# Performance work log

Hardware: AMD Instinct MI355X
Metric: run time of the kernel (lower is better)

The kernel has to match this reference:

```python
import jax, jax.numpy as jnp
import numpy as np

# video grid and attention geometry (must match init_kwargs)
F_T, H_T, W_T = 4, 32, 32
K = 3                      # kernel_size (odd)
P = K // 2
T = F_T * H_T * W_T        # max_num_tokens = 4096
HEADS = 8
DIM_HEAD = 64
SCALE = DIM_HEAD ** -0.5
DIM = 512
INNER = HEADS * DIM_HEAD


def _build_window_indices():
    # flat token index grid, padded with sentinel T (out-of-range -> zero row after gather)
    idx = np.arange(T).reshape(F_T, H_T, W_T)
    padded = np.full((F_T + 2 * P, H_T + 2 * P, W_T + 2 * P), T, dtype=np.int64)
    padded[P:P + F_T, P:P + H_T, P:P + W_T] = idx
    # [T, K^3] neighborhood indices, kernel offsets in (kf, kh, kw) C-order (matches unfoldNd)
    win = np.lib.stride_tricks.sliding_window_view(padded, (K, K, K)).reshape(T, K ** 3)
    # causal: mask keys whose flat index is strictly in the future of the query
    causal = np.arange(T)[:, None] < win
    causal = np.concatenate([np.zeros((T, 1), dtype=bool), causal], axis=1)  # BOS column never masked
    return jnp.asarray(win), jnp.asarray(causal)

WIN_IDX, CAUSAL_MASK = _build_window_indices()


def setup_inputs() -> dict:
    key = jax.random.key(0)
    k0, k1, k2, k3 = jax.random.split(key, 4)
    n = T  # 1 BOS + (T-1) video tokens; padding logic pads body to exactly T tokens
    x = jax.random.normal(k0, (2, n, DIM), dtype=jnp.float32)
    Wq = jax.random.normal(k1, (DIM, INNER), dtype=jnp.float32) * (DIM ** -0.5)
    Wkv = jax.random.normal(k2, (DIM, 2 * INNER), dtype=jnp.float32) * (DIM ** -0.5)
    Wo = jax.random.normal(k3, (INNER, DIM), dtype=jnp.float32) * (INNER ** -0.5)
    bo = jnp.zeros((DIM,), dtype=jnp.float32)
    return {"x": x, "Wq": Wq, "Wkv": Wkv, "Wo": Wo, "bo": bo}


def _split_heads(t, b):
    # [b, n, h*d] -> [(b*h), n, d]
    n = t.shape[1]
    return t.reshape(b, n, HEADS, DIM_HEAD).transpose(0, 2, 1, 3).reshape(b * HEADS, n, DIM_HEAD)


def reference(x, Wq, Wkv, Wo, bo):
    b, n, _ = x.shape
    tpf = H_T * W_T
    padding = tpf - (n - 1) % tpf  # pads body tokens to a multiple of tokens_per_frame
    x = jnp.pad(x, ((0, 0), (0, padding), (0, 0)))
    q = x @ Wq
    k, v = jnp.split(x @ Wkv, 2, axis=-1)
    q, k, v = (_split_heads(t, b) for t in (q, k, v))
    bh = b * HEADS
    q = q[:, 1:] * SCALE            # drop BOS query; [bh, T, d]
    bos_v = v[:, :1]                # BOS attends only to itself -> its value passes through
    k_bos, k = k[:, :1], k[:, 1:]
    v_bos, v = v[:, :1], v[:, 1:]
    # gather K^3 3D neighborhoods; sentinel index T maps to a zero row
    zero_row = jnp.zeros((bh, 1, DIM_HEAD), dtype=k.dtype)
    k_nb = jnp.concatenate([k, zero_row], axis=1)[:, WIN_IDX]   # [bh, T, K^3, d]
    v_nb = jnp.concatenate([v, zero_row], axis=1)[:, WIN_IDX]
    # prepend global BOS key/value to every window
    k_nb = jnp.concatenate([jnp.broadcast_to(k_bos[:, :, None], (bh, T, 1, DIM_HEAD)), k_nb], axis=2)
    v_nb = jnp.concatenate([jnp.broadcast_to(v_bos[:, :, None], (bh, T, 1, DIM_HEAD)), v_nb], axis=2)
    sim = jnp.einsum('bid,bijd->bij', q, k_nb)                  # [bh, T, K^3+1]
    sim = jnp.where(CAUSAL_MASK[None], -jnp.finfo(sim.dtype).max, sim)
    attn = jax.nn.softmax(sim, axis=-1)
    out = jnp.einsum('bij,bijd->bid', attn, v_nb)               # [bh, T, d]
    out = jnp.concatenate([bos_v, out], axis=1)                 # [bh, T+1, d]
    np_tok = out.shape[1]
    out = out.reshape(b, HEADS, np_tok, DIM_HEAD).transpose(0, 2, 1, 3).reshape(b, np_tok, INNER)
    return (out @ Wo + bo)[:, :n]
```

## Files before the change

kernel.cpp:

```cpp
#include <hip/hip_runtime.h>


#define T_TOK   4096
#define DIM     512
#define NQKV    1536

typedef unsigned short u16;
typedef unsigned int   u32;
typedef unsigned long long u64;
typedef __attribute__((ext_vector_type(8))) short short8;
typedef __attribute__((ext_vector_type(4))) float f32x4;

__device__ __forceinline__ u16 f2bf(float f) {
    u32 u = __float_as_uint(f);
    return (u16)((u + 0x7fffu + ((u >> 16) & 1u)) >> 16);
}
__device__ __forceinline__ float b2f(u16 u) {
    return __uint_as_float(((u32)u) << 16);
}

__device__ __forceinline__ void gload_lds16(const void* g, void* l) {
    __builtin_amdgcn_global_load_lds(
        (const __attribute__((address_space(1))) void*)g,
        (__attribute__((address_space(3))) void*)l, 16, 0, 0);
}

__global__ void cast_all_kernel(const float4* __restrict__ x,
                                const float* __restrict__ Wq, const float* __restrict__ Wkv,
                                const float* __restrict__ Wo,
                                u16* __restrict__ xb, u16* __restrict__ Wt,
                                u16* __restrict__ Wot) {
    __shared__ float S[64 * 65];
    int blk = blockIdx.x;
    int tid = threadIdx.x;
    if (blk < 4096) {
        int i = blk * 256 + tid;
        float4 v = x[i];
        u64 pack = (u64)f2bf(v.x) | ((u64)f2bf(v.y) << 16) |
                   ((u64)f2bf(v.z) << 32) | ((u64)f2bf(v.w) << 48);
        ((u64*)xb)[i] = pack;
        return;
    }
    int isWo = blk >= 4288;
    int tIdx = isWo ? (blk - 4288) : (blk - 4096);
    int tn = tIdx >> 3, tk = tIdx & 7;
    #pragma unroll
    for (int p = 0; p < 16; ++p) {
        int kl = p * 4 + (tid >> 6), nl = tid & 63;
        int gk = tk * 64 + kl, gn = tn * 64 + nl;
        float v;
        if (isWo)            v = Wo[gk * 512 + gn];
        else if (gn < 512)   v = Wq[gk * 512 + gn];
        else                 v = Wkv[gk * 1024 + (gn - 512)];
        S[kl * 65 + nl] = v;
    }
    __syncthreads();
    u16* dst = isWo ? Wot : Wt;
    #pragma unroll
    for (int p = 0; p < 16; ++p) {
        int nl = p * 4 + (tid >> 6), kl = tid & 63;
        dst[(size_t)(tn * 64 + nl) * 512 + tk * 64 + kl] = f2bf(S[kl * 65 + nl]);
    }
}

template <int BM, int BN, int MODE>
__global__ __launch_bounds__(256)
void gemm_nt(const u16* __restrict__ A, const u16* __restrict__ B,
             void* __restrict__ Cv, const float* __restrict__ bias,
             int lda, int ldb, int ldc) {
    constexpr int K = 512, BK = 32;
    constexpr int ACH = BM * 4;
    constexpr int NCH = (BM + BN) * 4;
    constexpr int NLD = NCH / 256;
    constexpr int ABYTES = BM * 64;
    constexpr int MI = BM / 32, NJ = BN / 32;
    __shared__ __align__(16) char lds[(BM + BN) * 64];
    const int tid  = threadIdx.x;
    const int lane = tid & 63, wave = tid >> 6;
    const int quad = lane >> 4, mrow = lane & 15;
    const int wm = wave >> 1, wn = wave & 1;
    const int bm = blockIdx.y, bn = blockIdx.x;

    const char* gptr[NLD];
    char*       lptr[NLD];
    #pragma unroll
    for (int it = 0; it < NLD; ++it) {
        int c   = it * 256 + tid;
        int inB = (c >= ACH);
        int a   = inB ? c - ACH : c;
        int r   = a >> 2;
        int kc  = ((a & 3) - (r >> 1)) & 3;
        int row = (inB ? bn * BN : bm * BM) + r;
        const u16* base = inB ? B : A;
        int ld = inB ? ldb : lda;
        gptr[it] = (const char*)(base + (size_t)row * ld + kc * 8);
        lptr[it] = (char*)lds + (it * 256 + wave * 64) * 16;
    }
    const short8* aLds[MI];
    const short8* bLds[NJ];
    #pragma unroll
    for (int i = 0; i < MI; ++i) {
        int ra = wm * (BM / 2) + i * 16 + mrow;
        aLds[i] = (const short8*)(lds + (ra * 4 + ((quad + (ra >> 1)) & 3)) * 16);
    }
    #pragma unroll
    for (int j = 0; j < NJ; ++j) {
        int rb = wn * (BN / 2) + j * 16 + mrow;
        bLds[j] = (const short8*)(lds + ABYTES + (rb * 4 + ((quad + (rb >> 1)) & 3)) * 16);
    }

    f32x4 acc[MI][NJ] = {};
    for (int k0 = 0; k0 < K; k0 += BK) {
        #pragma unroll
        for (int it = 0; it < NLD; ++it)
            gload_lds16(gptr[it] + 2 * k0, lptr[it]);
        __syncthreads();
        short8 af[MI], bf[NJ];
        #pragma unroll
        for (int i = 0; i < MI; ++i) af[i] = *aLds[i];
        #pragma unroll
        for (int j = 0; j < NJ; ++j) bf[j] = *bLds[j];
        #pragma unroll
        for (int i = 0; i < MI; ++i)
            #pragma unroll
            for (int j = 0; j < NJ; ++j)
                acc[i][j] = __builtin_amdgcn_mfma_f32_16x16x32_bf16(af[i], bf[j], acc[i][j], 0, 0, 0);
        __syncthreads();
    }

    #pragma unroll
    for (int i = 0; i < MI; ++i) {
        #pragma unroll
        for (int j = 0; j < NJ; ++j) {
            int colg = bn * BN + wn * (BN / 2) + j * 16 + mrow;
            #pragma unroll
            for (int r = 0; r < 4; ++r) {
                int rowg = bm * BM + wm * (BM / 2) + i * 16 + quad * 4 + r;
                if (MODE == 0) {
                    ((u16*)Cv)[(size_t)rowg * ldc + colg] = f2bf(acc[i][j][r]);
                } else {
                    ((float*)Cv)[(size_t)rowg * ldc + colg] = acc[i][j][r] + bias[colg];
                }
            }
        }
    }
}

__global__ __launch_bounds__(256)
void attn_kernel(const u16* __restrict__ QKV, u16* __restrict__ O) {
    const int wid  = blockIdx.x * 4 + (threadIdx.x >> 6);
    const int lane = threadIdx.x & 63;
    const int bh = wid >> 12;
    const int ti = wid & 4095;
    const int b = bh >> 3, h = bh & 7;
    const size_t baseQ = (size_t)b * T_TOK * NQKV;
    const size_t baseO = (size_t)b * T_TOK * DIM;

    if (ti == 0) {
        O[baseO + h * 64 + lane] = QKV[baseQ + 1024 + h * 64 + lane];
        return;
    }
    const int t = ti - 1;
    const int f = t >> 10, hh = (t >> 5) & 31, ww = t & 31;

    const int j = lane >> 2, g = lane & 3;
    int jm1 = j - 1;
    int dh9 = ((jm1 * 11) >> 5) - 1;
    int dw9 = jm1 - (dh9 + 1) * 3 - 1;
    int df = (j >= 1 && j <= 9) ? -1 : 0;
    int dh = (j >= 1 && j <= 9) ? dh9 : ((j >= 10 && j <= 12) ? -1 : 0);
    int dw = (j >= 1 && j <= 9) ? dw9 :
             ((j >= 10 && j <= 12) ? (j - 11) : ((j == 13) ? -1 : 0));
    int nf = f + df, nh = hh + dh, nw = ww + dw;
    int valid = (nf >= 0) && ((unsigned)nh < 32u) && ((unsigned)nw < 32u)
                && (j >= 1) && (j <= 14);
    int p = valid ? (t + 1 + df * 1024 + dh * 32 + dw) : 0;
    int score_on = valid || (j == 0);

    const u16* qrow = QKV + baseQ + (size_t)(t + 1) * NQKV + h * 64 + g * 16;
    short8 q0 = *(const short8*)qrow;
    short8 q1 = *(const short8*)(qrow + 8);
    const u16* krow = QKV + baseQ + (size_t)p * NQKV + 512 + h * 64 + g * 16;
    short8 k0 = *(const short8*)krow;
    short8 k1 = *(const short8*)(krow + 8);
    float s = 0.f;
    #pragma unroll
    for (int i = 0; i < 8; ++i) {
        s = fmaf(b2f((u16)q0[i]), b2f((u16)k0[i]), s);
        s = fmaf(b2f((u16)q1[i]), b2f((u16)k1[i]), s);
    }
    s += __shfl_xor(s, 1);
    s += __shfl_xor(s, 2);
    s *= 0.125f;
    s = score_on ? s : -3.0e38f;

    float m = s;
    #pragma unroll
    for (int off = 4; off <= 32; off <<= 1) m = fmaxf(m, __shfl_xor(m, off));
    float pe = __expf(s - m);
    float l = pe;
    #pragma unroll
    for (int off = 4; off <= 32; off <<= 1) l += __shfl_xor(l, off);
    float pen = pe * __frcp_rn(l);
    u32 voff = (u32)p * 3072u;

    float acc = 0.f;
    const char* vb = (const char*)(QKV + baseQ + 1024 + h * 64 + lane);
    #pragma unroll
    for (int jj = 0; jj < 15; ++jj) {
        u32 o = (u32)__builtin_amdgcn_readlane((int)voff, jj * 4);
        float pj = __uint_as_float(
                     (u32)__builtin_amdgcn_readlane((int)__float_as_uint(pen), jj * 4));
        float vv = b2f(*(const u16*)(vb + o));
        acc = fmaf(pj, vv, acc);
    }
    O[baseO + (size_t)ti * DIM + h * 64 + lane] = f2bf(acc);
}

extern "C" void kernel_launch(void* const* d_in, const int* in_sizes, int n_in,
                              void* d_out, int out_size, void* d_ws, size_t ws_size,
                              hipStream_t stream) {
    const float* x   = (const float*)d_in[0];
    const float* Wq  = (const float*)d_in[1];
    const float* Wkv = (const float*)d_in[2];
    const float* Wo  = (const float*)d_in[3];
    const float* bo  = (const float*)d_in[4];
    float* out = (float*)d_out;
    char* ws = (char*)d_ws;

    u16* xb  = (u16*)(ws + 0);
    u16* Wt  = (u16*)(ws + 8388608);
    u16* Wot = (u16*)(ws + 9961472);
    u16* QKV = (u16*)(ws + 10485760);
    u16* O   = (u16*)(ws + 0);

    cast_all_kernel<<<dim3(4352), dim3(256), 0, stream>>>(
        (const float4*)x, Wq, Wkv, Wo, xb, Wt, Wot);
    gemm_nt<128, 128, 0><<<dim3(12, 64), dim3(256), 0, stream>>>(
        xb, Wt, (void*)QKV, nullptr, 512, 512, 1536);
    attn_kernel<<<dim3(16384), dim3(256), 0, stream>>>(QKV, O);
    gemm_nt<128, 64, 1><<<dim3(8, 64), dim3(256), 0, stream>>>(
        O, Wot, (void*)out, bo, 512, 512, 512);
}
```

Measured before the change: 147.9 us.

## Replace LDS-staged GEMM with direct global-to-register loads and register prefetch

Result: slower. 182.7 us (+23.5%).

```diff
diff --git a/kernel.cpp b/kernel.cpp
--- a/kernel.cpp
+++ b/kernel.cpp
@@ -17,12 +17,6 @@
 }
 __device__ __forceinline__ float b2f(u16 u) {
     return __uint_as_float(((u32)u) << 16);
-}
-
-__device__ __forceinline__ void gload_lds16(const void* g, void* l) {
-    __builtin_amdgcn_global_load_lds(
-        (const __attribute__((address_space(1))) void*)g,
-        (__attribute__((address_space(3))) void*)l, 16, 0, 0);
 }
 
 __global__ void cast_all_kernel(const float4* __restrict__ x,
@@ -64,68 +58,54 @@
 }
 
 template <int BM, int BN, int MODE>
-__global__ __launch_bounds__(256)
-void gemm_nt(const u16* __restrict__ A, const u16* __restrict__ B,
-             void* __restrict__ Cv, const float* __restrict__ bias,
-             int lda, int ldb, int ldc) {
-    constexpr int K = 512, BK = 32;
-    constexpr int ACH = BM * 4;
-    constexpr int NCH = (BM + BN) * 4;
-    constexpr int NLD = NCH / 256;
-    constexpr int ABYTES = BM * 64;
+__global__ __launch_bounds__(256, 3)
+void gemm_direct(const u16* __restrict__ A, const u16* __restrict__ B,
+                 void* __restrict__ Cv, const float* __restrict__ bias,
+                 int lda, int ldb, int ldc) {
+    constexpr int KSTEPS = 16;
     constexpr int MI = BM / 32, NJ = BN / 32;
-    __shared__ __align__(16) char lds[(BM + BN) * 64];
-    const int tid  = threadIdx.x;
-    const int lane = tid & 63, wave = tid >> 6;
+    const int lane = threadIdx.x & 63, wave = threadIdx.x >> 6;
     const int quad = lane >> 4, mrow = lane & 15;
     const int wm = wave >> 1, wn = wave & 1;
     const int bm = blockIdx.y, bn = blockIdx.x;
 
-    const char* gptr[NLD];
-    char*       lptr[NLD];
-    #pragma unroll
-    for (int it = 0; it < NLD; ++it) {
-        int c   = it * 256 + tid;
-        int inB = (c >= ACH);
-        int a   = inB ? c - ACH : c;
-        int r   = a >> 2;
-        int kc  = ((a & 3) - (r >> 1)) & 3;
-        int row = (inB ? bn * BN : bm * BM) + r;
-        const u16* base = inB ? B : A;
-        int ld = inB ? ldb : lda;
-        gptr[it] = (const char*)(base + (size_t)row * ld + kc * 8);
-        lptr[it] = (char*)lds + (it * 256 + wave * 64) * 16;
-    }
-    const short8* aLds[MI];
-    const short8* bLds[NJ];
+    const short8* aP[MI];
+    const short8* bP[NJ];
     #pragma unroll
     for (int i = 0; i < MI; ++i) {
-        int ra = wm * (BM / 2) + i * 16 + mrow;
-        aLds[i] = (const short8*)(lds + (ra * 4 + ((quad + (ra >> 1)) & 3)) * 16);
+        int row = bm * BM + wm * (BM / 2) + i * 16 + mrow;
+        aP[i] = (const short8*)(A + (size_t)row * lda + quad * 8);
     }
     #pragma unroll
     for (int j = 0; j < NJ; ++j) {
-        int rb = wn * (BN / 2) + j * 16 + mrow;
-        bLds[j] = (const short8*)(lds + ABYTES + (rb * 4 + ((quad + (rb >> 1)) & 3)) * 16);
+        int row = bn * BN + wn * (BN / 2) + j * 16 + mrow;
+        bP[j] = (const short8*)(B + (size_t)row * ldb + quad * 8);
     }
 
     f32x4 acc[MI][NJ] = {};
-    for (int k0 = 0; k0 < K; k0 += BK) {
-        #pragma unroll
-        for (int it = 0; it < NLD; ++it)
-            gload_lds16(gptr[it] + 2 * k0, lptr[it]);
-        __syncthreads();
-        short8 af[MI], bf[NJ];
-        #pragma unroll
-        for (int i = 0; i < MI; ++i) af[i] = *aLds[i];
-        #pragma unroll
-        for (int j = 0; j < NJ; ++j) bf[j] = *bLds[j];
+    short8 aC[MI], bC[NJ], aN[MI], bN[NJ];
+    #pragma unroll
+    for (int i = 0; i < MI; ++i) aC[i] = aP[i][0];
+    #pragma unroll
+    for (int j = 0; j < NJ; ++j) bC[j] = bP[j][0];
+
+    #pragma unroll 4
+    for (int ks = 0; ks < KSTEPS; ++ks) {
+        if (ks + 1 < KSTEPS) {
+            #pragma unroll
+            for (int i = 0; i < MI; ++i) aN[i] = aP[i][(ks + 1) * 4];
+            #pragma unroll
+            for (int j = 0; j < NJ; ++j) bN[j] = bP[j][(ks + 1) * 4];
+        }
         #pragma unroll
         for (int i = 0; i < MI; ++i)
             #pragma unroll
             for (int j = 0; j < NJ; ++j)
-                acc[i][j] = __builtin_amdgcn_mfma_f32_16x16x32_bf16(af[i], bf[j], acc[i][j], 0, 0, 0);
-        __syncthreads();
+                acc[i][j] = __builtin_amdgcn_mfma_f32_16x16x32_bf16(aC[i], bC[j], acc[i][j], 0, 0, 0);
+        #pragma unroll
+        for (int i = 0; i < MI; ++i) aC[i] = aN[i];
+        #pragma unroll
+        for (int j = 0; j < NJ; ++j) bC[j] = bN[j];
     }
 
     #pragma unroll
@@ -236,9 +216,9 @@
 
     cast_all_kernel<<<dim3(4352), dim3(256), 0, stream>>>(
         (const float4*)x, Wq, Wkv, Wo, xb, Wt, Wot);
-    gemm_nt<128, 128, 0><<<dim3(12, 64), dim3(256), 0, stream>>>(
+    gemm_direct<128, 128, 0><<<dim3(12, 64), dim3(256), 0, stream>>>(
         xb, Wt, (void*)QKV, nullptr, 512, 512, 1536);
     attn_kernel<<<dim3(16384), dim3(256), 0, stream>>>(QKV, O);
-    gemm_nt<128, 64, 1><<<dim3(8, 64), dim3(256), 0, stream>>>(
+    gemm_direct<128, 64, 1><<<dim3(8, 64), dim3(256), 0, stream>>>(
         O, Wot, (void*)out, bo, 512, 512, 512);
 }
```

## Double-buffer GEMM LDS tiles to overlap global loads with MFMA compute

Applied to the files above, without the earlier changes.

Measured after the change: 138.8 us. -6.2%, faster.

```diff
diff --git a/kernel.cpp b/kernel.cpp
--- a/kernel.cpp
+++ b/kernel.cpp
@@ -68,13 +68,14 @@
 void gemm_nt(const u16* __restrict__ A, const u16* __restrict__ B,
              void* __restrict__ Cv, const float* __restrict__ bias,
              int lda, int ldb, int ldc) {
-    constexpr int K = 512, BK = 32;
+    constexpr int K = 512, BK = 32, KSTEPS = K / BK;
     constexpr int ACH = BM * 4;
     constexpr int NCH = (BM + BN) * 4;
     constexpr int NLD = NCH / 256;
     constexpr int ABYTES = BM * 64;
+    constexpr int HALF = (BM + BN) * 64;
     constexpr int MI = BM / 32, NJ = BN / 32;
-    __shared__ __align__(16) char lds[(BM + BN) * 64];
+    __shared__ __align__(16) char lds[2 * HALF];
     const int tid  = threadIdx.x;
     const int lane = tid & 63, wave = tid >> 6;
     const int quad = lane >> 4, mrow = lane & 15;
@@ -96,36 +97,49 @@
         gptr[it] = (const char*)(base + (size_t)row * ld + kc * 8);
         lptr[it] = (char*)lds + (it * 256 + wave * 64) * 16;
     }
-    const short8* aLds[MI];
-    const short8* bLds[NJ];
+    const char* aLds[MI];
+    const char* bLds[NJ];
     #pragma unroll
     for (int i = 0; i < MI; ++i) {
         int ra = wm * (BM / 2) + i * 16 + mrow;
-        aLds[i] = (const short8*)(lds + (ra * 4 + ((quad + (ra >> 1)) & 3)) * 16);
+        aLds[i] = lds + (ra * 4 + ((quad + (ra >> 1)) & 3)) * 16;
     }
     #pragma unroll
     for (int j = 0; j < NJ; ++j) {
         int rb = wn * (BN / 2) + j * 16 + mrow;
-        bLds[j] = (const short8*)(lds + ABYTES + (rb * 4 + ((quad + (rb >> 1)) & 3)) * 16);
+        bLds[j] = lds + ABYTES + (rb * 4 + ((quad + (rb >> 1)) & 3)) * 16;
     }
 
     f32x4 acc[MI][NJ] = {};
-    for (int k0 = 0; k0 < K; k0 += BK) {
-        #pragma unroll
-        for (int it = 0; it < NLD; ++it)
-            gload_lds16(gptr[it] + 2 * k0, lptr[it]);
-        __syncthreads();
+    #pragma unroll
+    for (int it = 0; it < NLD; ++it)
+        gload_lds16(gptr[it], lptr[it]);
+
+    #pragma unroll
+    for (int ks = 0; ks < KSTEPS; ++ks) {
+        const int cur = ks & 1;
+        if (ks + 1 < KSTEPS) {
+            #pragma unroll
+            for (int it = 0; it < NLD; ++it)
+                gload_lds16(gptr[it] + 2 * (ks + 1) * BK, lptr[it] + (cur ^ 1) * HALF);
+            asm volatile("s_waitcnt vmcnt(%0)" :: "i"(NLD) : "memory");
+        } else {
+            asm volatile("s_waitcnt vmcnt(0)" ::: "memory");
+        }
+        asm volatile("s_barrier" ::: "memory");
+
         short8 af[MI], bf[NJ];
         #pragma unroll
-        for (int i = 0; i < MI; ++i) af[i] = *aLds[i];
-        #pragma unroll
-        for (int j = 0; j < NJ; ++j) bf[j] = *bLds[j];
+        for (int i = 0; i < MI; ++i) af[i] = *(const short8*)(aLds[i] + cur * HALF);
+        #pragma unroll
+        for (int j = 0; j < NJ; ++j) bf[j] = *(const short8*)(bLds[j] + cur * HALF);
         #pragma unroll
         for (int i = 0; i < MI; ++i)
             #pragma unroll
             for (int j = 0; j < NJ; ++j)
                 acc[i][j] = __builtin_amdgcn_mfma_f32_16x16x32_bf16(af[i], bf[j], acc[i][j], 0, 0, 0);
-        __syncthreads();
+        asm volatile("s_waitcnt lgkmcnt(0)" ::: "memory");
+        asm volatile("s_barrier" ::: "memory");
     }
 
     #pragma unroll
```
